# Performance work log

Measured on AMD Instinct MI355X. Metric: run time of the kernel, lower is better.

Reference implementation:

```python
import jax, jax.numpy as jnp
import numpy as np

B, T, N, F_IN, F_OUT, K = 16, 12, 1024, 64, 64, 3


def setup_inputs() -> dict:
    key = jax.random.key(0)
    k1, k2, k3, k4 = jax.random.split(key, 4)
    x = jax.random.normal(k1, (B, T, N, F_IN), dtype=jnp.float32)
    spatial_attention = jax.random.uniform(k2, (B, N, N), dtype=jnp.float32)
    cheb = jax.random.normal(k3, (K, N, N), dtype=jnp.float32) / np.sqrt(N)
    # Xavier-uniform-ish init for Theta [K, F_in, F_out]
    limit = np.sqrt(6.0 / (F_IN + F_OUT))
    Theta = jax.random.uniform(k4, (K, F_IN, F_OUT), dtype=jnp.float32,
                               minval=-limit, maxval=limit)
    return {"x": x, "spatial_attention": spatial_attention, "cheb": cheb, "Theta": Theta}


def reference(x, spatial_attention, cheb, Theta):
    # Attention-weighted Chebyshev adjacencies: [B, K, N, N]
    A = cheb[None, :, :, :] * spatial_attention[:, None, :, :]
    # Graph propagation for all t, k at once: [B, T, K, N, F_in]
    rhs = jnp.einsum('bkij,btjf->btkif', A, x)
    # Per-order linear map + sum over K: [B, T, N, F_out]
    out = jnp.einsum('btkif,kfo->btio', rhs, Theta)
    return jax.nn.relu(out)
```

## Files before the change

### kernel.cpp

```cpp
#include <hip/hip_runtime.h>
#include <hip/hip_bf16.h>

#define BB 16
#define TT 12
#define NN 1024
#define FF 64
#define KC 3

typedef __bf16  bf16x8 __attribute__((ext_vector_type(8)));
typedef float   f32x4  __attribute__((ext_vector_type(4)));
typedef float   f32x16 __attribute__((ext_vector_type(16)));
typedef unsigned short u16;

#define A_TILE 24576
#define Y_TILE 32768
#define MFMA_B(a, b, c) __builtin_amdgcn_mfma_f32_32x32x16_bf16(a, b, c, 0, 0, 0)

#define YF_BYTES 25165824ull
#define CB_BYTES 6291456ull

static __device__ __forceinline__ u16 f2bf(float v) {
    union { __bf16 b; u16 u; } c; c.b = (__bf16)v; return c.u;
}

static __device__ __forceinline__ void load_lds16(const void* g, void* l) {
    __builtin_amdgcn_global_load_lds(
        (const __attribute__((address_space(1))) unsigned int*)g,
        (__attribute__((address_space(3))) unsigned int*)l, 16, 0, 0);
}

__global__ __launch_bounds__(256) void x_to_yfrags(
    const float* __restrict__ x, u16* __restrict__ y)
{
    __shared__ char tl[64 * 128];
    const int tid = threadIdx.x;
    const int bt  = blockIdx.x >> 4;
    const int jt  = blockIdx.x & 15;
    const int f   = tid & 63;
    const int jr  = tid >> 6;

    const float* xp = x + ((size_t)bt * NN + jt * 64 + jr) * FF + f;
    #pragma unroll
    for (int stp = 0; stp < 16; ++stp) {
        int j = stp * 4 + jr;
        u16 h = f2bf(xp[stp * 4 * FF]);
        *reinterpret_cast<u16*>(tl + j * 128 + ((f * 2) ^ ((j & 7) << 4))) = h;
    }
    __syncthreads();

    u16* yo = y + ((size_t)bt * 16 + jt) * 4096;
    #pragma unroll
    for (int p = 0; p < 2; ++p) {
        int c  = tid + p * 256;
        int s  = c >> 6, fo = c & 63;
        int j0 = (s >> 1) * 16 + (s & 1) * 8;
        u16 h[8];
        #pragma unroll
        for (int e = 0; e < 8; ++e)
            h[e] = *reinterpret_cast<u16*>(tl + (j0 + e) * 128 + ((fo * 2) ^ (e << 4)));
        uint4 w;
        w.x = h[0] | ((unsigned)h[1] << 16);
        w.y = h[2] | ((unsigned)h[3] << 16);
        w.z = h[4] | ((unsigned)h[5] << 16);
        w.w = h[6] | ((unsigned)h[7] << 16);
        *reinterpret_cast<uint4*>(yo + (size_t)c * 8) = w;
    }
}

__global__ __launch_bounds__(256) void cheb_to_bf16(
    const float* __restrict__ c, u16* __restrict__ o)
{
    const size_t i = ((size_t)blockIdx.x * 256 + threadIdx.x) * 8;
    f32x4 a = *reinterpret_cast<const f32x4*>(c + i);
    f32x4 b = *reinterpret_cast<const f32x4*>(c + i + 4);
    u16 h[8];
    #pragma unroll
    for (int e = 0; e < 4; ++e) { h[e] = f2bf(a[e]); h[e + 4] = f2bf(b[e]); }
    uint4 w;
    w.x = h[0] | ((unsigned)h[1] << 16);
    w.y = h[2] | ((unsigned)h[3] << 16);
    w.z = h[4] | ((unsigned)h[5] << 16);
    w.w = h[6] | ((unsigned)h[7] << 16);
    *reinterpret_cast<uint4*>(o + i) = w;
}

__global__ __launch_bounds__(512, 1) void cheb_main(
    const u16*  __restrict__ yfr,
    const float* __restrict__ att,
    const u16*  __restrict__ chb,
    const float* __restrict__ Theta,
    float* __restrict__ out)
{
    __shared__ __align__(16) char lds[2 * A_TILE + 2 * Y_TILE];
    char* Ab0 = lds;
    char* Ab1 = lds + A_TILE;
    char* Yb0 = lds + 2 * A_TILE;
    char* Yb1 = Yb0 + Y_TILE;

    const int tid  = threadIdx.x;
    const int lane = tid & 63;
    const int wid  = tid >> 6;

    const int wg = (blockIdx.x & 7) * 96 + (blockIdx.x >> 3);
    const int b  = wg / 48;
    const int it = (wg % 48) / 3;
    const int tc = wg % 3;
    const int i_base = it * 64;
    const int t_base = tc * 4;

    const int wm  = wid >> 1;
    const int wn  = wid & 1;
    const int l31 = lane & 31;
    const int lg  = lane >> 5;
    const int sw3 = (l31 >> 2) & 7;

    const int r_a = tid >> 3;
    const int g_a = tid & 7;
    const int swza_st = ((r_a >> 2) & 7) << 4;
    const float* attR = att + ((size_t)b * NN + i_base + r_a) * NN + g_a * 8;
    const u16*   chR  = chb + ((size_t)(i_base + r_a)) * NN + g_a * 8;

    f32x16 acc[KC][2] = {};
    const int arow = (wn * 32 + l31) * 128;

    f32x4 ra0, ra1;
    bf16x8 rc[KC];

    auto LOADS = [&](int j0) {
        ra0 = *reinterpret_cast<const f32x4*>(attR + j0);
        ra1 = *reinterpret_cast<const f32x4*>(attR + j0 + 4);
        #pragma unroll
        for (int k = 0; k < KC; ++k)
            rc[k] = *reinterpret_cast<const bf16x8*>(chR + (size_t)k * NN * NN + j0);
    };
    auto FINISH = [&](char* Ab) {
        #pragma unroll
        for (int k = 0; k < KC; ++k) {
            bf16x8 w;
            #pragma unroll
            for (int e = 0; e < 4; ++e) {
                w[e]     = (__bf16)(ra0[e] * (float)rc[k][e]);
                w[e + 4] = (__bf16)(ra1[e] * (float)rc[k][e + 4]);
            }
            *reinterpret_cast<bf16x8*>(
                Ab + (k * 64 + r_a) * 128 + ((g_a * 16) ^ swza_st)) = w;
        }
    };

    auto loadY_lds = [&](char* Yb, int jt) {
        #pragma unroll
        for (int q = 0; q < 4; ++q) {
            int s    = wid * 4 + q;
            int tile = s >> 3;
            int part = s & 7;
            const u16* gp = yfr + ((size_t)(b * TT + t_base + tile) * 16 + jt) * 4096
                          + (size_t)(part * 64 + lane) * 8;
            load_lds16(gp, Yb + tile * 8192 + part * 1024);
        }
    };

    auto phase4 = [&](const char* Abase, const char* Ybase) {
        const char* yt = Ybase + wm * 8192;
        #pragma unroll
        for (int kk = 0; kk < 4; ++kk) {
            const int off  = ((kk * 2 + lg) ^ sw3) << 4;
            const int yoff = (kk * 2 + lg) * 1024 + l31 * 16;
            bf16x8 af0 = *reinterpret_cast<const bf16x8*>(yt + yoff);
            bf16x8 af1 = *reinterpret_cast<const bf16x8*>(yt + yoff + 512);
            bf16x8 b0 = *reinterpret_cast<const bf16x8*>(Abase + arow + off);
            bf16x8 b1 = *reinterpret_cast<const bf16x8*>(Abase + 8192 + arow + off);
            bf16x8 b2 = *reinterpret_cast<const bf16x8*>(Abase + 16384 + arow + off);
            __builtin_amdgcn_s_setprio(1);
            acc[0][0] = MFMA_B(af0, b0, acc[0][0]); acc[0][1] = MFMA_B(af1, b0, acc[0][1]);
            acc[1][0] = MFMA_B(af0, b1, acc[1][0]); acc[1][1] = MFMA_B(af1, b1, acc[1][1]);
            acc[2][0] = MFMA_B(af0, b2, acc[2][0]); acc[2][1] = MFMA_B(af1, b2, acc[2][1]);
            __builtin_amdgcn_s_setprio(0);
        }
    };

    auto body = [&](char* curA, char* altA, char* curY, char* altY, int jt) {
        loadY_lds(altY, (jt + 1) & 15);
        __builtin_amdgcn_sched_barrier(0);
        phase4(curA, curY);
        if (jt < 15) {
            FINISH(altA);
            LOADS(((jt + 2) & 15) * 64);
        }
        asm volatile("s_waitcnt vmcnt(5)" ::: "memory");
        asm volatile("s_waitcnt lgkmcnt(0)" ::: "memory");
        __builtin_amdgcn_s_barrier();
    };

    loadY_lds(Yb0, 0);
    LOADS(0);
    asm volatile("s_waitcnt vmcnt(0)" ::: "memory");
    FINISH(Ab0);
    LOADS(64);
    asm volatile("s_waitcnt lgkmcnt(0)" ::: "memory");
    __builtin_amdgcn_s_barrier();

    #pragma unroll 1
    for (int h = 0; h < 8; ++h) {
        body(Ab0, Ab1, Yb0, Yb1, 2 * h);
        body(Ab1, Ab0, Yb1, Yb0, 2 * h + 1);
    }

    {
        const int fi0 = wid * 3;
        #pragma unroll
        for (int q = 0; q < 3; ++q) {
            int fi = fi0 + q;
            int k  = fi >> 3;
            int mo = (fi >> 2) & 1;
            int s  = fi & 3;
            int o  = 32 * mo + l31;
            int fb = 32 * (s >> 1) + 16 * (s & 1) + 4 * lg;
            bf16x8 v;
            #pragma unroll
            for (int e = 0; e < 8; ++e) {
                int f = fb + (e & 3) + 8 * (e >> 2);
                v[e] = (__bf16)Theta[(k * FF + f) * FF + o];
            }
            *reinterpret_cast<bf16x8*>(lds + (fi * 64 + lane) * 16) = v;
        }
    }
    __syncthreads();

    f32x16 of[2] = {};
    #pragma unroll
    for (int k = 0; k < KC; ++k) {
        #pragma unroll
        for (int s = 0; s < 4; ++s) {
            bf16x8 pb;
            #pragma unroll
            for (int e = 0; e < 8; ++e)
                pb[e] = (__bf16)acc[k][s >> 1][e + 8 * (s & 1)];
            #pragma unroll
            for (int mo = 0; mo < 2; ++mo) {
                bf16x8 th = *reinterpret_cast<const bf16x8*>(
                    lds + ((((k * 2 + mo) * 4 + s) * 64) + lane) * 16);
                of[mo] = MFMA_B(pb, th, of[mo]);
            }
        }
    }

    const int t = t_base + wm;
    float* op = out + (((size_t)b * TT + t) * NN + i_base + wn * 32) * FF;
    #pragma unroll
    for (int mo = 0; mo < 2; ++mo) {
        #pragma unroll
        for (int r = 0; r < 16; ++r) {
            int row = (r & 3) + 8 * (r >> 2) + 4 * lg;
            int o   = 32 * mo + l31;
            float v = of[mo][r];
            op[(size_t)row * FF + o] = v > 0.0f ? v : 0.0f;
        }
    }
}

__global__ __launch_bounds__(512, 2) void cheb_fused(
    const float* __restrict__ x, const float* __restrict__ att,
    const float* __restrict__ cheb, const float* __restrict__ Theta,
    float* __restrict__ out)
{
    __shared__ __align__(16) char lds_raw[2 * (A_TILE + 32768)];
    char* Ab0 = lds_raw;
    char* Xb0 = lds_raw + A_TILE;
    char* Ab1 = lds_raw + A_TILE + 32768;
    char* Xb1 = Ab1 + A_TILE;

    const int tid  = threadIdx.x;
    const int lane = tid & 63;
    const int wid  = tid >> 6;
    const int wg = (blockIdx.x & 7) * 96 + (blockIdx.x >> 3);
    const int b  = wg / 48;
    const int it = (wg % 48) / 3;
    const int tc = wg % 3;
    const int i_base = it * 64;
    const int t_base = tc * 4;
    const int wm  = wid >> 1;
    const int wn  = wid & 1;
    const int l31 = lane & 31;
    const int lg  = lane >> 5;
    const int sw3 = (l31 >> 2) & 7;
    const float* attB = att + (size_t)b * NN * NN;
    const float* xB   = x + (size_t)b * TT * NN * FF;
    const int r_a = tid >> 3;
    const int g_a = tid & 7;
    const int swza_st = ((r_a >> 2) & 7) << 4;
    int tl_s[4], jj_s[4], f_s[4], swzx_st[4];
    #pragma unroll
    for (int s = 0; s < 4; ++s) {
        int u = tid + s * 512;
        tl_s[s] = u >> 9;
        int rem = u & 511;
        jj_s[s] = (rem >> 4) * 2;
        f_s[s]  = (rem & 15) * 4;
        swzx_st[s] = ((f_s[s] >> 2) & 7) << 4;
    }
    f32x4 ra0, ra1, rc0[KC], rc1[KC], rx0[4], rx1[4];
    auto load_tile = [&](int j0) {
        const float* ap = attB + (size_t)(i_base + r_a) * NN + j0 + g_a * 8;
        ra0 = *reinterpret_cast<const f32x4*>(ap);
        ra1 = *reinterpret_cast<const f32x4*>(ap + 4);
        #pragma unroll
        for (int k = 0; k < KC; ++k) {
            const float* cp = cheb + ((size_t)k * NN + i_base + r_a) * NN + j0 + g_a * 8;
            rc0[k] = *reinterpret_cast<const f32x4*>(cp);
            rc1[k] = *reinterpret_cast<const f32x4*>(cp + 4);
        }
        #pragma unroll
        for (int s = 0; s < 4; ++s) {
            const float* xp = xB + ((size_t)(t_base + tl_s[s]) * NN + j0 + jj_s[s]) * FF + f_s[s];
            rx0[s] = *reinterpret_cast<const f32x4*>(xp);
            rx1[s] = *reinterpret_cast<const f32x4*>(xp + FF);
        }
    };
    auto store_A = [&](char* Ab) {
        #pragma unroll
        for (int k = 0; k < KC; ++k) {
            bf16x8 w;
            #pragma unroll
            for (int e = 0; e < 4; ++e) {
                w[e]     = (__bf16)(rc0[k][e] * ra0[e]);
                w[e + 4] = (__bf16)(rc1[k][e] * ra1[e]);
            }
            *reinterpret_cast<bf16x8*>(Ab + (k * 64 + r_a) * 128 + ((g_a * 16) ^ swza_st)) = w;
        }
    };
    auto store_X = [&](char* Xb) {
        #pragma unroll
        for (int s = 0; s < 4; ++s) {
            const int c0 = tl_s[s] * 64 + f_s[s];
            const int coloff = (jj_s[s] * 2) ^ swzx_st[s];
            #pragma unroll
            for (int e = 0; e < 4; ++e) {
                union { __bf16 h[2]; unsigned u32; } pk;
                pk.h[0] = (__bf16)rx0[s][e];
                pk.h[1] = (__bf16)rx1[s][e];
                *reinterpret_cast<unsigned*>(Xb + (c0 + e) * 128 + coloff) = pk.u32;
            }
        }
    };
    f32x16 acc[KC][2] = {};
    const int xrow0 = (wm * 64 + l31) * 128;
    const int xrow1 = xrow0 + 32 * 128;
    const int arow  = (wn * 32 + l31) * 128;
    auto phase = [&](const char* AbR, const char* XbR, int kk) {
        const int off = ((kk * 2 + lg) ^ sw3) << 4;
        bf16x8 af0 = *reinterpret_cast<const bf16x8*>(XbR + xrow0 + off);
        bf16x8 af1 = *reinterpret_cast<const bf16x8*>(XbR + xrow1 + off);
        bf16x8 b0  = *reinterpret_cast<const bf16x8*>(AbR + arow + off);
        bf16x8 b1  = *reinterpret_cast<const bf16x8*>(AbR + 8192 + arow + off);
        bf16x8 b2  = *reinterpret_cast<const bf16x8*>(AbR + 16384 + arow + off);
        __builtin_amdgcn_s_setprio(1);
        acc[0][0] = MFMA_B(af0, b0, acc[0][0]); acc[0][1] = MFMA_B(af1, b0, acc[0][1]);
        acc[1][0] = MFMA_B(af0, b1, acc[1][0]); acc[1][1] = MFMA_B(af1, b1, acc[1][1]);
        acc[2][0] = MFMA_B(af0, b2, acc[2][0]); acc[2][1] = MFMA_B(af1, b2, acc[2][1]);
        __builtin_amdgcn_s_setprio(0);
    };
    load_tile(0);
    store_A(Ab0);
    store_X(Xb0);
    load_tile(64);
    asm volatile("s_waitcnt lgkmcnt(0)" ::: "memory");
    __builtin_amdgcn_s_barrier();
    for (int jt2 = 0; jt2 < 8; ++jt2) {
        const int jt = jt2 * 2;
        phase(Ab0, Xb0, 0);
        phase(Ab0, Xb0, 1);
        store_A(Ab1);
        phase(Ab0, Xb0, 2);
        store_X(Xb1);
        phase(Ab0, Xb0, 3);
        if (jt + 2 < 16) load_tile((jt + 2) * 64);
        asm volatile("s_waitcnt lgkmcnt(0)" ::: "memory");
        __builtin_amdgcn_s_barrier();
        phase(Ab1, Xb1, 0);
        phase(Ab1, Xb1, 1);
        if (jt + 1 < 15) store_A(Ab0);
        phase(Ab1, Xb1, 2);
        if (jt + 1 < 15) store_X(Xb0);
        phase(Ab1, Xb1, 3);
        if (jt + 3 < 16) load_tile((jt + 3) * 64);
        asm volatile("s_waitcnt lgkmcnt(0)" ::: "memory");
        __builtin_amdgcn_s_barrier();
    }
    {
        const int fi0 = wid * 3;
        #pragma unroll
        for (int q = 0; q < 3; ++q) {
            int fi = fi0 + q;
            int k  = fi >> 3;
            int mo = (fi >> 2) & 1;
            int s  = fi & 3;
            int o  = 32 * mo + l31;
            int fb = 32 * (s >> 1) + 16 * (s & 1) + 4 * lg;
            bf16x8 v;
            #pragma unroll
            for (int e = 0; e < 8; ++e) {
                int f = fb + (e & 3) + 8 * (e >> 2);
                v[e] = (__bf16)Theta[(k * FF + f) * FF + o];
            }
            *reinterpret_cast<bf16x8*>(lds_raw + (fi * 64 + lane) * 16) = v;
        }
    }
    __syncthreads();
    f32x16 of[2] = {};
    #pragma unroll
    for (int k = 0; k < KC; ++k) {
        #pragma unroll
        for (int s = 0; s < 4; ++s) {
            bf16x8 pb;
            #pragma unroll
            for (int e = 0; e < 8; ++e)
                pb[e] = (__bf16)acc[k][s >> 1][e + 8 * (s & 1)];
            #pragma unroll
            for (int mo = 0; mo < 2; ++mo) {
                bf16x8 th = *reinterpret_cast<const bf16x8*>(
                    lds_raw + ((((k * 2 + mo) * 4 + s) * 64) + lane) * 16);
                of[mo] = MFMA_B(pb, th, of[mo]);
            }
        }
    }
    const int t = t_base + wm;
    float* op = out + (((size_t)b * TT + t) * NN + i_base + wn * 32) * FF;
    #pragma unroll
    for (int mo = 0; mo < 2; ++mo) {
        #pragma unroll
        for (int r = 0; r < 16; ++r) {
            int row = (r & 3) + 8 * (r >> 2) + 4 * lg;
            int o   = 32 * mo + l31;
            float v = of[mo][r];
            op[(size_t)row * FF + o] = v > 0.0f ? v : 0.0f;
        }
    }
}

extern "C" void kernel_launch(void* const* d_in, const int* in_sizes, int n_in,
                              void* d_out, int out_size, void* d_ws, size_t ws_size,
                              hipStream_t stream) {
    const float* x     = (const float*)d_in[0];
    const float* att   = (const float*)d_in[1];
    const float* cheb  = (const float*)d_in[2];
    const float* Theta = (const float*)d_in[3];
    float* out = (float*)d_out;
    (void)in_sizes; (void)n_in; (void)out_size;

    if (ws_size >= YF_BYTES + CB_BYTES) {
        u16* yfr = (u16*)d_ws;
        u16* cbf = (u16*)((char*)d_ws + YF_BYTES);
        x_to_yfrags<<<dim3(BB * TT * 16), 256, 0, stream>>>(x, yfr);
        cheb_to_bf16<<<dim3(KC * NN * NN / (256 * 8)), 256, 0, stream>>>(cheb, cbf);
        cheb_main<<<dim3(BB * 16 * 3), 512, 0, stream>>>(yfr, att, cbf, Theta, out);
    } else {
        cheb_fused<<<dim3(BB * 16 * 3), 512, 0, stream>>>(x, att, cheb, Theta, out);
    }
}
```

Before: 105.9 us.

## Precompute attention-weighted Chebyshev tiles in a separate kernel and DMA them

```diff
diff --git a/kernel.cpp b/kernel.cpp
--- a/kernel.cpp
+++ b/kernel.cpp
@@ -17,7 +17,10 @@
 #define MFMA_B(a, b, c) __builtin_amdgcn_mfma_f32_32x32x16_bf16(a, b, c, 0, 0, 0)
 
 #define YF_BYTES 25165824ull
+#define AW_BYTES 100663296ull
 #define CB_BYTES 6291456ull
+#define T1_BYTES (YF_BYTES + AW_BYTES)
+#define T2_BYTES (YF_BYTES + CB_BYTES)
 
 static __device__ __forceinline__ u16 f2bf(float v) {
     union { __bf16 b; u16 u; } c; c.b = (__bf16)v; return c.u;
@@ -67,27 +70,51 @@
     }
 }
 
-__global__ __launch_bounds__(256) void cheb_to_bf16(
-    const float* __restrict__ c, u16* __restrict__ o)
+__global__ __launch_bounds__(256) void build_A(
+    const float* __restrict__ att, const float* __restrict__ cheb,
+    u16* __restrict__ aw)
 {
-    const size_t i = ((size_t)blockIdx.x * 256 + threadIdx.x) * 8;
-    f32x4 a = *reinterpret_cast<const f32x4*>(c + i);
-    f32x4 b = *reinterpret_cast<const f32x4*>(c + i + 4);
-    u16 h[8];
-    #pragma unroll
-    for (int e = 0; e < 4; ++e) { h[e] = f2bf(a[e]); h[e + 4] = f2bf(b[e]); }
-    uint4 w;
-    w.x = h[0] | ((unsigned)h[1] << 16);
-    w.y = h[2] | ((unsigned)h[3] << 16);
-    w.z = h[4] | ((unsigned)h[5] << 16);
-    w.w = h[6] | ((unsigned)h[7] << 16);
-    *reinterpret_cast<uint4*>(o + i) = w;
-}
-
-__global__ __launch_bounds__(512, 1) void cheb_main(
+    const int bid = blockIdx.x;
+    const int b  = bid & 15;
+    const int it = (bid >> 4) & 15;
+    const int jt = bid >> 8;
+    const int tid = threadIdx.x;
+    const int row = tid >> 2;
+    const int jg2 = tid & 3;
+
+    const float* ap = att + ((size_t)b * NN + it * 64 + row) * NN + jt * 64 + jg2 * 16;
+    f32x4 a0 = *reinterpret_cast<const f32x4*>(ap);
+    f32x4 a1 = *reinterpret_cast<const f32x4*>(ap + 4);
+    f32x4 a2 = *reinterpret_cast<const f32x4*>(ap + 8);
+    f32x4 a3 = *reinterpret_cast<const f32x4*>(ap + 12);
+
+    char* tw = (char*)aw + ((size_t)(b * 16 + it) * 16 + jt) * A_TILE;
+    const int key = ((row >> 2) & 7) << 4;
+
+    #pragma unroll
+    for (int k = 0; k < KC; ++k) {
+        const float* cp = cheb + ((size_t)k * NN + it * 64 + row) * NN + jt * 64 + jg2 * 16;
+        f32x4 c0 = *reinterpret_cast<const f32x4*>(cp);
+        f32x4 c1 = *reinterpret_cast<const f32x4*>(cp + 4);
+        f32x4 c2 = *reinterpret_cast<const f32x4*>(cp + 8);
+        f32x4 c3 = *reinterpret_cast<const f32x4*>(cp + 12);
+        bf16x8 w0, w1;
+        #pragma unroll
+        for (int e = 0; e < 4; ++e) {
+            w0[e]     = (__bf16)(a0[e] * c0[e]);
+            w0[e + 4] = (__bf16)(a1[e] * c1[e]);
+            w1[e]     = (__bf16)(a2[e] * c2[e]);
+            w1[e + 4] = (__bf16)(a3[e] * c3[e]);
+        }
+        char* rb = tw + k * 8192 + row * 128;
+        *reinterpret_cast<bf16x8*>(rb + (((jg2 * 2) << 4) ^ key))     = w0;
+        *reinterpret_cast<bf16x8*>(rb + (((jg2 * 2 + 1) << 4) ^ key)) = w1;
+    }
+}
+
+__global__ __launch_bounds__(512, 1) void cheb_main_t1(
     const u16*  __restrict__ yfr,
-    const float* __restrict__ att,
-    const u16*  __restrict__ chb,
+    const u16*  __restrict__ aw,
     const float* __restrict__ Theta,
     float* __restrict__ out)
 {
@@ -114,40 +141,20 @@
     const int lg  = lane >> 5;
     const int sw3 = (l31 >> 2) & 7;
 
-    const int r_a = tid >> 3;
-    const int g_a = tid & 7;
-    const int swza_st = ((r_a >> 2) & 7) << 4;
-    const float* attR = att + ((size_t)b * NN + i_base + r_a) * NN + g_a * 8;
-    const u16*   chR  = chb + ((size_t)(i_base + r_a)) * NN + g_a * 8;
-
     f32x16 acc[KC][2] = {};
     const int arow = (wn * 32 + l31) * 128;
 
-    f32x4 ra0, ra1;
-    bf16x8 rc[KC];
-
-    auto LOADS = [&](int j0) {
-        ra0 = *reinterpret_cast<const f32x4*>(attR + j0);
-        ra1 = *reinterpret_cast<const f32x4*>(attR + j0 + 4);
-        #pragma unroll
-        for (int k = 0; k < KC; ++k)
-            rc[k] = *reinterpret_cast<const bf16x8*>(chR + (size_t)k * NN * NN + j0);
-    };
-    auto FINISH = [&](char* Ab) {
-        #pragma unroll
-        for (int k = 0; k < KC; ++k) {
-            bf16x8 w;
-            #pragma unroll
-            for (int e = 0; e < 4; ++e) {
-                w[e]     = (__bf16)(ra0[e] * (float)rc[k][e]);
-                w[e + 4] = (__bf16)(ra1[e] * (float)rc[k][e + 4]);
-            }
-            *reinterpret_cast<bf16x8*>(
-                Ab + (k * 64 + r_a) * 128 + ((g_a * 16) ^ swza_st)) = w;
-        }
-    };
-
-    auto loadY_lds = [&](char* Yb, int jt) {
+    const char* aT0 = (const char*)aw + ((size_t)(b * 16 + it) * 16) * A_TILE;
+
+    auto dmaA = [&](char* Ab, int jt) {
+        const char* src = aT0 + (size_t)jt * A_TILE;
+        #pragma unroll
+        for (int q = 0; q < 3; ++q) {
+            int seg = wid * 3 + q;
+            load_lds16(src + seg * 1024 + lane * 16, Ab + seg * 1024 + lane * 16);
+        }
+    };
+    auto dmaY = [&](char* Yb, int jt) {
         #pragma unroll
         for (int q = 0; q < 4; ++q) {
             int s    = wid * 4 + q;
@@ -178,31 +185,26 @@
         }
     };
 
-    auto body = [&](char* curA, char* altA, char* curY, char* altY, int jt) {
-        loadY_lds(altY, (jt + 1) & 15);
+    dmaA(Ab0, 0);
+    dmaY(Yb0, 0);
+    asm volatile("s_waitcnt vmcnt(0)" ::: "memory");
+    __builtin_amdgcn_s_barrier();
+
+    #pragma unroll 1
+    for (int jt = 0; jt < 16; ++jt) {
+        char* curA = (jt & 1) ? Ab1 : Ab0;
+        char* altA = (jt & 1) ? Ab0 : Ab1;
+        char* curY = (jt & 1) ? Yb1 : Yb0;
+        char* altY = (jt & 1) ? Yb0 : Yb1;
+        if (jt < 15) {
+            dmaA(altA, jt + 1);
+            dmaY(altY, jt + 1);
+        }
         __builtin_amdgcn_sched_barrier(0);
         phase4(curA, curY);
-        if (jt < 15) {
-            FINISH(altA);
-            LOADS(((jt + 2) & 15) * 64);
-        }
-        asm volatile("s_waitcnt vmcnt(5)" ::: "memory");
+        asm volatile("s_waitcnt vmcnt(0)" ::: "memory");
         asm volatile("s_waitcnt lgkmcnt(0)" ::: "memory");
         __builtin_amdgcn_s_barrier();
-    };
-
-    loadY_lds(Yb0, 0);
-    LOADS(0);
-    asm volatile("s_waitcnt vmcnt(0)" ::: "memory");
-    FINISH(Ab0);
-    LOADS(64);
-    asm volatile("s_waitcnt lgkmcnt(0)" ::: "memory");
-    __builtin_amdgcn_s_barrier();
-
-    #pragma unroll 1
-    for (int h = 0; h < 8; ++h) {
-        body(Ab0, Ab1, Yb0, Yb1, 2 * h);
-        body(Ab1, Ab0, Yb1, Yb0, 2 * h + 1);
     }
 
     {
@@ -244,6 +246,187 @@
         }
     }
 
+    const int t = t_base + wm;
+    float* op = out + (((size_t)b * TT + t) * NN + i_base + wn * 32) * FF;
+    #pragma unroll
+    for (int mo = 0; mo < 2; ++mo) {
+        #pragma unroll
+        for (int r = 0; r < 16; ++r) {
+            int row = (r & 3) + 8 * (r >> 2) + 4 * lg;
+            int o   = 32 * mo + l31;
+            float v = of[mo][r];
+            op[(size_t)row * FF + o] = v > 0.0f ? v : 0.0f;
+        }
+    }
+}
+
+__global__ __launch_bounds__(256) void cheb_to_bf16(
+    const float* __restrict__ c, u16* __restrict__ o)
+{
+    const size_t i = ((size_t)blockIdx.x * 256 + threadIdx.x) * 8;
+    f32x4 a = *reinterpret_cast<const f32x4*>(c + i);
+    f32x4 b = *reinterpret_cast<const f32x4*>(c + i + 4);
+    u16 h[8];
+    #pragma unroll
+    for (int e = 0; e < 4; ++e) { h[e] = f2bf(a[e]); h[e + 4] = f2bf(b[e]); }
+    uint4 w;
+    w.x = h[0] | ((unsigned)h[1] << 16);
+    w.y = h[2] | ((unsigned)h[3] << 16);
+    w.z = h[4] | ((unsigned)h[5] << 16);
+    w.w = h[6] | ((unsigned)h[7] << 16);
+    *reinterpret_cast<uint4*>(o + i) = w;
+}
+
+__global__ __launch_bounds__(512, 1) void cheb_main_t2(
+    const u16*  __restrict__ yfr, const float* __restrict__ att,
+    const u16*  __restrict__ chb, const float* __restrict__ Theta,
+    float* __restrict__ out)
+{
+    __shared__ __align__(16) char lds[2 * A_TILE + 2 * Y_TILE];
+    char* Ab0 = lds;
+    char* Ab1 = lds + A_TILE;
+    char* Yb0 = lds + 2 * A_TILE;
+    char* Yb1 = Yb0 + Y_TILE;
+
+    const int tid  = threadIdx.x;
+    const int lane = tid & 63;
+    const int wid  = tid >> 6;
+    const int wg = (blockIdx.x & 7) * 96 + (blockIdx.x >> 3);
+    const int b  = wg / 48;
+    const int it = (wg % 48) / 3;
+    const int tc = wg % 3;
+    const int i_base = it * 64;
+    const int t_base = tc * 4;
+    const int wm  = wid >> 1;
+    const int wn  = wid & 1;
+    const int l31 = lane & 31;
+    const int lg  = lane >> 5;
+    const int sw3 = (l31 >> 2) & 7;
+    const int r_a = tid >> 3;
+    const int g_a = tid & 7;
+    const int swza_st = ((r_a >> 2) & 7) << 4;
+    const float* attR = att + ((size_t)b * NN + i_base + r_a) * NN + g_a * 8;
+    const u16*   chR  = chb + ((size_t)(i_base + r_a)) * NN + g_a * 8;
+
+    f32x16 acc[KC][2] = {};
+    const int arow = (wn * 32 + l31) * 128;
+    f32x4 ra0, ra1;
+    bf16x8 rc[KC];
+
+    auto LOADS = [&](int j0) {
+        ra0 = *reinterpret_cast<const f32x4*>(attR + j0);
+        ra1 = *reinterpret_cast<const f32x4*>(attR + j0 + 4);
+        #pragma unroll
+        for (int k = 0; k < KC; ++k)
+            rc[k] = *reinterpret_cast<const bf16x8*>(chR + (size_t)k * NN * NN + j0);
+    };
+    auto FINISH = [&](char* Ab) {
+        #pragma unroll
+        for (int k = 0; k < KC; ++k) {
+            bf16x8 w;
+            #pragma unroll
+            for (int e = 0; e < 4; ++e) {
+                w[e]     = (__bf16)(ra0[e] * (float)rc[k][e]);
+                w[e + 4] = (__bf16)(ra1[e] * (float)rc[k][e + 4]);
+            }
+            *reinterpret_cast<bf16x8*>(Ab + (k * 64 + r_a) * 128 + ((g_a * 16) ^ swza_st)) = w;
+        }
+    };
+    auto loadY_lds = [&](char* Yb, int jt) {
+        #pragma unroll
+        for (int q = 0; q < 4; ++q) {
+            int s    = wid * 4 + q;
+            int tile = s >> 3;
+            int part = s & 7;
+            const u16* gp = yfr + ((size_t)(b * TT + t_base + tile) * 16 + jt) * 4096
+                          + (size_t)(part * 64 + lane) * 8;
+            load_lds16(gp, Yb + tile * 8192 + part * 1024);
+        }
+    };
+    auto phase4 = [&](const char* Abase, const char* Ybase) {
+        const char* yt = Ybase + wm * 8192;
+        #pragma unroll
+        for (int kk = 0; kk < 4; ++kk) {
+            const int off  = ((kk * 2 + lg) ^ sw3) << 4;
+            const int yoff = (kk * 2 + lg) * 1024 + l31 * 16;
+            bf16x8 af0 = *reinterpret_cast<const bf16x8*>(yt + yoff);
+            bf16x8 af1 = *reinterpret_cast<const bf16x8*>(yt + yoff + 512);
+            bf16x8 b0 = *reinterpret_cast<const bf16x8*>(Abase + arow + off);
+            bf16x8 b1 = *reinterpret_cast<const bf16x8*>(Abase + 8192 + arow + off);
+            bf16x8 b2 = *reinterpret_cast<const bf16x8*>(Abase + 16384 + arow + off);
+            __builtin_amdgcn_s_setprio(1);
+            acc[0][0] = MFMA_B(af0, b0, acc[0][0]); acc[0][1] = MFMA_B(af1, b0, acc[0][1]);
+            acc[1][0] = MFMA_B(af0, b1, acc[1][0]); acc[1][1] = MFMA_B(af1, b1, acc[1][1]);
+            acc[2][0] = MFMA_B(af0, b2, acc[2][0]); acc[2][1] = MFMA_B(af1, b2, acc[2][1]);
+            __builtin_amdgcn_s_setprio(0);
+        }
+    };
+
+    auto body = [&](char* curA, char* altA, char* curY, char* altY, int jt) {
+        loadY_lds(altY, (jt + 1) & 15);
+        __builtin_amdgcn_sched_barrier(0);
+        phase4(curA, curY);
+        if (jt < 15) {
+            FINISH(altA);
+            LOADS(((jt + 2) & 15) * 64);
+        }
+        asm volatile("s_waitcnt vmcnt(5)" ::: "memory");
+        asm volatile("s_waitcnt lgkmcnt(0)" ::: "memory");
+        __builtin_amdgcn_s_barrier();
+    };
+
+    loadY_lds(Yb0, 0);
+    LOADS(0);
+    asm volatile("s_waitcnt vmcnt(0)" ::: "memory");
+    FINISH(Ab0);
+    LOADS(64);
+    asm volatile("s_waitcnt lgkmcnt(0)" ::: "memory");
+    __builtin_amdgcn_s_barrier();
+
+    #pragma unroll 1
+    for (int h = 0; h < 8; ++h) {
+        body(Ab0, Ab1, Yb0, Yb1, 2 * h);
+        body(Ab1, Ab0, Yb1, Yb0, 2 * h + 1);
+    }
+
+    {
+        const int fi0 = wid * 3;
+        #pragma unroll
+        for (int q = 0; q < 3; ++q) {
+            int fi = fi0 + q;
+            int k  = fi >> 3;
+            int mo = (fi >> 2) & 1;
+            int s  = fi & 3;
+            int o  = 32 * mo + l31;
+            int fb = 32 * (s >> 1) + 16 * (s & 1) + 4 * lg;
+            bf16x8 v;
+            #pragma unroll
+            for (int e = 0; e < 8; ++e) {
+                int f = fb + (e & 3) + 8 * (e >> 2);
+                v[e] = (__bf16)Theta[(k * FF + f) * FF + o];
+            }
+            *reinterpret_cast<bf16x8*>(lds + (fi * 64 + lane) * 16) = v;
+        }
+    }
+    __syncthreads();
+
+    f32x16 of[2] = {};
+    #pragma unroll
+    for (int k = 0; k < KC; ++k) {
+        #pragma unroll
+        for (int s = 0; s < 4; ++s) {
+            bf16x8 pb;
+            #pragma unroll
+            for (int e = 0; e < 8; ++e)
+                pb[e] = (__bf16)acc[k][s >> 1][e + 8 * (s & 1)];
+            #pragma unroll
+            for (int mo = 0; mo < 2; ++mo) {
+                bf16x8 th = *reinterpret_cast<const bf16x8*>(
+                    lds + ((((k * 2 + mo) * 4 + s) * 64) + lane) * 16);
+                of[mo] = MFMA_B(pb, th, of[mo]);
+            }
+        }
+    }
     const int t = t_base + wm;
     float* op = out + (((size_t)b * TT + t) * NN + i_base + wn * 32) * FF;
     #pragma unroll
@@ -447,12 +630,18 @@
     float* out = (float*)d_out;
     (void)in_sizes; (void)n_in; (void)out_size;
 
-    if (ws_size >= YF_BYTES + CB_BYTES) {
+    if (ws_size >= T1_BYTES) {
+        u16* yfr = (u16*)d_ws;
+        u16* aw  = (u16*)((char*)d_ws + YF_BYTES);
+        x_to_yfrags<<<dim3(BB * TT * 16), 256, 0, stream>>>(x, yfr);
+        build_A<<<dim3(16 * 16 * 16), 256, 0, stream>>>(att, cheb, aw);
+        cheb_main_t1<<<dim3(BB * 16 * 3), 512, 0, stream>>>(yfr, aw, Theta, out);
+    } else if (ws_size >= T2_BYTES) {
         u16* yfr = (u16*)d_ws;
         u16* cbf = (u16*)((char*)d_ws + YF_BYTES);
         x_to_yfrags<<<dim3(BB * TT * 16), 256, 0, stream>>>(x, yfr);
         cheb_to_bf16<<<dim3(KC * NN * NN / (256 * 8)), 256, 0, stream>>>(cheb, cbf);
-        cheb_main<<<dim3(BB * 16 * 3), 512, 0, stream>>>(yfr, att, cbf, Theta, out);
+        cheb_main_t2<<<dim3(BB * 16 * 3), 512, 0, stream>>>(yfr, att, cbf, Theta, out);
     } else {
         cheb_fused<<<dim3(BB * 16 * 3), 512, 0, stream>>>(x, att, cheb, Theta, out);
     }
```

Result: slower. 158.1 us (+49.2%).

## Widen main kernel workgroup to six timesteps to reuse attention-weighted Chebyshev tiles

Applied to the files above, without the earlier changes.

```diff
diff --git a/kernel.cpp b/kernel.cpp
--- a/kernel.cpp
+++ b/kernel.cpp
@@ -12,12 +12,15 @@
 typedef float   f32x16 __attribute__((ext_vector_type(16)));
 typedef unsigned short u16;
 
-#define A_TILE 24576
-#define Y_TILE 32768
+#define A_TILE  24576
+#define A_ROWB  144
+#define A_TILEP (KC * 64 * A_ROWB)
+#define Y_HEX   (6 * 8192)
 #define MFMA_B(a, b, c) __builtin_amdgcn_mfma_f32_32x32x16_bf16(a, b, c, 0, 0, 0)
 
 #define YF_BYTES 25165824ull
 #define CB_BYTES 6291456ull
+#define T2_BYTES (YF_BYTES + CB_BYTES)
 
 static __device__ __forceinline__ u16 f2bf(float v) {
     union { __bf16 b; u16 u; } c; c.b = (__bf16)v; return c.u;
@@ -84,44 +87,44 @@
     *reinterpret_cast<uint4*>(o + i) = w;
 }
 
-__global__ __launch_bounds__(512, 1) void cheb_main(
+__global__ __launch_bounds__(768, 3) void cheb_main_hex(
     const u16*  __restrict__ yfr,
     const float* __restrict__ att,
     const u16*  __restrict__ chb,
     const float* __restrict__ Theta,
     float* __restrict__ out)
 {
-    __shared__ __align__(16) char lds[2 * A_TILE + 2 * Y_TILE];
+    __shared__ __align__(16) char lds[2 * A_TILEP + 2 * Y_HEX];
     char* Ab0 = lds;
-    char* Ab1 = lds + A_TILE;
-    char* Yb0 = lds + 2 * A_TILE;
-    char* Yb1 = Yb0 + Y_TILE;
+    char* Ab1 = lds + A_TILEP;
+    char* Yb0 = lds + 2 * A_TILEP;
+    char* Yb1 = Yb0 + Y_HEX;
 
     const int tid  = threadIdx.x;
     const int lane = tid & 63;
     const int wid  = tid >> 6;
-
-    const int wg = (blockIdx.x & 7) * 96 + (blockIdx.x >> 3);
-    const int b  = wg / 48;
-    const int it = (wg % 48) / 3;
-    const int tc = wg % 3;
+    const bool staging = (wid < 8);
+
+    const int wg = (blockIdx.x & 7) * 64 + (blockIdx.x >> 3);
+    const int b  = wg >> 5;
+    const int rm = wg & 31;
+    const int it = rm >> 1;
+    const int th = rm & 1;
     const int i_base = it * 64;
-    const int t_base = tc * 4;
-
-    const int wm  = wid >> 1;
-    const int wn  = wid & 1;
+    const int t0     = th * 6;
+
+    const int wn    = wid / 6;
+    const int t_loc = wid % 6;
     const int l31 = lane & 31;
     const int lg  = lane >> 5;
-    const int sw3 = (l31 >> 2) & 7;
 
     const int r_a = tid >> 3;
     const int g_a = tid & 7;
-    const int swza_st = ((r_a >> 2) & 7) << 4;
     const float* attR = att + ((size_t)b * NN + i_base + r_a) * NN + g_a * 8;
     const u16*   chR  = chb + ((size_t)(i_base + r_a)) * NN + g_a * 8;
 
     f32x16 acc[KC][2] = {};
-    const int arow = (wn * 32 + l31) * 128;
+    const int arow = (wn * 32 + l31) * A_ROWB;
 
     f32x4 ra0, ra1;
     bf16x8 rc[KC];
@@ -142,34 +145,32 @@
                 w[e]     = (__bf16)(ra0[e] * (float)rc[k][e]);
                 w[e + 4] = (__bf16)(ra1[e] * (float)rc[k][e + 4]);
             }
-            *reinterpret_cast<bf16x8*>(
-                Ab + (k * 64 + r_a) * 128 + ((g_a * 16) ^ swza_st)) = w;
-        }
-    };
-
-    auto loadY_lds = [&](char* Yb, int jt) {
+            *reinterpret_cast<bf16x8*>(Ab + (k * 64 + r_a) * A_ROWB + g_a * 16) = w;
+        }
+    };
+    auto dmaY = [&](char* Yb, int jt) {
         #pragma unroll
         for (int q = 0; q < 4; ++q) {
             int s    = wid * 4 + q;
             int tile = s >> 3;
             int part = s & 7;
-            const u16* gp = yfr + ((size_t)(b * TT + t_base + tile) * 16 + jt) * 4096
+            const u16* gp = yfr + ((size_t)(b * TT + t0 + tile) * 16 + jt) * 4096
                           + (size_t)(part * 64 + lane) * 8;
             load_lds16(gp, Yb + tile * 8192 + part * 1024);
         }
     };
 
     auto phase4 = [&](const char* Abase, const char* Ybase) {
-        const char* yt = Ybase + wm * 8192;
+        const char* yt = Ybase + t_loc * 8192;
         #pragma unroll
         for (int kk = 0; kk < 4; ++kk) {
-            const int off  = ((kk * 2 + lg) ^ sw3) << 4;
+            const int off  = (kk * 2 + lg) * 16;
             const int yoff = (kk * 2 + lg) * 1024 + l31 * 16;
             bf16x8 af0 = *reinterpret_cast<const bf16x8*>(yt + yoff);
             bf16x8 af1 = *reinterpret_cast<const bf16x8*>(yt + yoff + 512);
             bf16x8 b0 = *reinterpret_cast<const bf16x8*>(Abase + arow + off);
-            bf16x8 b1 = *reinterpret_cast<const bf16x8*>(Abase + 8192 + arow + off);
-            bf16x8 b2 = *reinterpret_cast<const bf16x8*>(Abase + 16384 + arow + off);
+            bf16x8 b1 = *reinterpret_cast<const bf16x8*>(Abase + 64 * A_ROWB + arow + off);
+            bf16x8 b2 = *reinterpret_cast<const bf16x8*>(Abase + 128 * A_ROWB + arow + off);
             __builtin_amdgcn_s_setprio(1);
             acc[0][0] = MFMA_B(af0, b0, acc[0][0]); acc[0][1] = MFMA_B(af1, b0, acc[0][1]);
             acc[1][0] = MFMA_B(af0, b1, acc[1][0]); acc[1][1] = MFMA_B(af1, b1, acc[1][1]);
@@ -178,37 +179,46 @@
         }
     };
 
-    auto body = [&](char* curA, char* altA, char* curY, char* altY, int jt) {
-        loadY_lds(altY, (jt + 1) & 15);
+    if (staging) {
+        LOADS(0);
+    }
+    dmaY(Yb0, 0);
+    if (staging) {
+        FINISH(Ab0);
+        LOADS(64);
+        asm volatile("s_waitcnt vmcnt(5)" ::: "memory");
+    } else {
+        asm volatile("s_waitcnt vmcnt(0)" ::: "memory");
+    }
+    asm volatile("s_waitcnt lgkmcnt(0)" ::: "memory");
+    __builtin_amdgcn_s_barrier();
+
+    #pragma unroll 1
+    for (int jt = 0; jt < 16; ++jt) {
+        char* curA = (jt & 1) ? Ab1 : Ab0;
+        char* altA = (jt & 1) ? Ab0 : Ab1;
+        char* curY = (jt & 1) ? Yb1 : Yb0;
+        char* altY = (jt & 1) ? Yb0 : Yb1;
+        dmaY(altY, (jt + 1) & 15);
+        if (staging) {
+            FINISH(altA);
+            LOADS(((jt + 2) & 15) * 64);
+        }
         __builtin_amdgcn_sched_barrier(0);
         phase4(curA, curY);
-        if (jt < 15) {
-            FINISH(altA);
-            LOADS(((jt + 2) & 15) * 64);
-        }
-        asm volatile("s_waitcnt vmcnt(5)" ::: "memory");
+        if (staging) {
+            asm volatile("s_waitcnt vmcnt(5)" ::: "memory");
+        } else {
+            asm volatile("s_waitcnt vmcnt(0)" ::: "memory");
+        }
         asm volatile("s_waitcnt lgkmcnt(0)" ::: "memory");
         __builtin_amdgcn_s_barrier();
-    };
-
-    loadY_lds(Yb0, 0);
-    LOADS(0);
-    asm volatile("s_waitcnt vmcnt(0)" ::: "memory");
-    FINISH(Ab0);
-    LOADS(64);
-    asm volatile("s_waitcnt lgkmcnt(0)" ::: "memory");
-    __builtin_amdgcn_s_barrier();
-
-    #pragma unroll 1
-    for (int h = 0; h < 8; ++h) {
-        body(Ab0, Ab1, Yb0, Yb1, 2 * h);
-        body(Ab1, Ab0, Yb1, Yb0, 2 * h + 1);
     }
 
     {
-        const int fi0 = wid * 3;
-        #pragma unroll
-        for (int q = 0; q < 3; ++q) {
+        const int fi0 = wid * 2;
+        #pragma unroll
+        for (int q = 0; q < 2; ++q) {
             int fi = fi0 + q;
             int k  = fi >> 3;
             int mo = (fi >> 2) & 1;
@@ -244,7 +254,7 @@
         }
     }
 
-    const int t = t_base + wm;
+    const int t = t0 + t_loc;
     float* op = out + (((size_t)b * TT + t) * NN + i_base + wn * 32) * FF;
     #pragma unroll
     for (int mo = 0; mo < 2; ++mo) {
@@ -447,12 +457,12 @@
     float* out = (float*)d_out;
     (void)in_sizes; (void)n_in; (void)out_size;
 
-    if (ws_size >= YF_BYTES + CB_BYTES) {
+    if (ws_size >= T2_BYTES) {
         u16* yfr = (u16*)d_ws;
         u16* cbf = (u16*)((char*)d_ws + YF_BYTES);
         x_to_yfrags<<<dim3(BB * TT * 16), 256, 0, stream>>>(x, yfr);
         cheb_to_bf16<<<dim3(KC * NN * NN / (256 * 8)), 256, 0, stream>>>(cheb, cbf);
-        cheb_main<<<dim3(BB * 16 * 3), 512, 0, stream>>>(yfr, att, cbf, Theta, out);
+        cheb_main_hex<<<dim3(BB * 16 * 2), 768, 0, stream>>>(yfr, att, cbf, Theta, out);
     } else {
         cheb_fused<<<dim3(BB * 16 * 3), 512, 0, stream>>>(x, att, cheb, Theta, out);
     }
```

Result: slower. 110.1 us (+3.9%).

## Triple-buffer Y tiles and pad A rows instead of XOR swizzle

Applied to the files above, without the earlier changes.

```diff
diff --git a/kernel.cpp b/kernel.cpp
--- a/kernel.cpp
+++ b/kernel.cpp
@@ -12,12 +12,15 @@
 typedef float   f32x16 __attribute__((ext_vector_type(16)));
 typedef unsigned short u16;
 
-#define A_TILE 24576
-#define Y_TILE 32768
+#define A_TILE  24576
+#define A_ROWB  144
+#define A_TILEP (KC * 64 * A_ROWB)
+#define Y_TILE  32768
 #define MFMA_B(a, b, c) __builtin_amdgcn_mfma_f32_32x32x16_bf16(a, b, c, 0, 0, 0)
 
 #define YF_BYTES 25165824ull
 #define CB_BYTES 6291456ull
+#define T2_BYTES (YF_BYTES + CB_BYTES)
 
 static __device__ __forceinline__ u16 f2bf(float v) {
     union { __bf16 b; u16 u; } c; c.b = (__bf16)v; return c.u;
@@ -84,18 +87,14 @@
     *reinterpret_cast<uint4*>(o + i) = w;
 }
 
-__global__ __launch_bounds__(512, 1) void cheb_main(
+__global__ __launch_bounds__(512, 1) void cheb_main_t2(
     const u16*  __restrict__ yfr,
     const float* __restrict__ att,
     const u16*  __restrict__ chb,
     const float* __restrict__ Theta,
     float* __restrict__ out)
 {
-    __shared__ __align__(16) char lds[2 * A_TILE + 2 * Y_TILE];
-    char* Ab0 = lds;
-    char* Ab1 = lds + A_TILE;
-    char* Yb0 = lds + 2 * A_TILE;
-    char* Yb1 = Yb0 + Y_TILE;
+    __shared__ __align__(16) char lds[2 * A_TILEP + 3 * Y_TILE];
 
     const int tid  = threadIdx.x;
     const int lane = tid & 63;
@@ -112,16 +111,14 @@
     const int wn  = wid & 1;
     const int l31 = lane & 31;
     const int lg  = lane >> 5;
-    const int sw3 = (l31 >> 2) & 7;
 
     const int r_a = tid >> 3;
     const int g_a = tid & 7;
-    const int swza_st = ((r_a >> 2) & 7) << 4;
     const float* attR = att + ((size_t)b * NN + i_base + r_a) * NN + g_a * 8;
     const u16*   chR  = chb + ((size_t)(i_base + r_a)) * NN + g_a * 8;
 
     f32x16 acc[KC][2] = {};
-    const int arow = (wn * 32 + l31) * 128;
+    const int arow = (wn * 32 + l31) * A_ROWB;
 
     f32x4 ra0, ra1;
     bf16x8 rc[KC];
@@ -133,7 +130,7 @@
         for (int k = 0; k < KC; ++k)
             rc[k] = *reinterpret_cast<const bf16x8*>(chR + (size_t)k * NN * NN + j0);
     };
-    auto FINISH = [&](char* Ab) {
+    auto FINISH = [&](int aOff) {
         #pragma unroll
         for (int k = 0; k < KC; ++k) {
             bf16x8 w;
@@ -142,12 +139,10 @@
                 w[e]     = (__bf16)(ra0[e] * (float)rc[k][e]);
                 w[e + 4] = (__bf16)(ra1[e] * (float)rc[k][e + 4]);
             }
-            *reinterpret_cast<bf16x8*>(
-                Ab + (k * 64 + r_a) * 128 + ((g_a * 16) ^ swza_st)) = w;
-        }
-    };
-
-    auto loadY_lds = [&](char* Yb, int jt) {
+            *reinterpret_cast<bf16x8*>(lds + aOff + (k * 64 + r_a) * A_ROWB + g_a * 16) = w;
+        }
+    };
+    auto dmaY = [&](int yOff, int jt) {
         #pragma unroll
         for (int q = 0; q < 4; ++q) {
             int s    = wid * 4 + q;
@@ -155,21 +150,22 @@
             int part = s & 7;
             const u16* gp = yfr + ((size_t)(b * TT + t_base + tile) * 16 + jt) * 4096
                           + (size_t)(part * 64 + lane) * 8;
-            load_lds16(gp, Yb + tile * 8192 + part * 1024);
-        }
-    };
-
-    auto phase4 = [&](const char* Abase, const char* Ybase) {
-        const char* yt = Ybase + wm * 8192;
+            load_lds16(gp, lds + yOff + tile * 8192 + part * 1024);
+        }
+    };
+
+    auto phase4 = [&](int aOff, int yOff) {
+        const char* yt = lds + yOff + wm * 8192;
+        const char* ab = lds + aOff;
         #pragma unroll
         for (int kk = 0; kk < 4; ++kk) {
-            const int off  = ((kk * 2 + lg) ^ sw3) << 4;
+            const int off  = (kk * 2 + lg) * 16;
             const int yoff = (kk * 2 + lg) * 1024 + l31 * 16;
             bf16x8 af0 = *reinterpret_cast<const bf16x8*>(yt + yoff);
             bf16x8 af1 = *reinterpret_cast<const bf16x8*>(yt + yoff + 512);
-            bf16x8 b0 = *reinterpret_cast<const bf16x8*>(Abase + arow + off);
-            bf16x8 b1 = *reinterpret_cast<const bf16x8*>(Abase + 8192 + arow + off);
-            bf16x8 b2 = *reinterpret_cast<const bf16x8*>(Abase + 16384 + arow + off);
+            bf16x8 b0 = *reinterpret_cast<const bf16x8*>(ab + arow + off);
+            bf16x8 b1 = *reinterpret_cast<const bf16x8*>(ab + 64 * A_ROWB + arow + off);
+            bf16x8 b2 = *reinterpret_cast<const bf16x8*>(ab + 128 * A_ROWB + arow + off);
             __builtin_amdgcn_s_setprio(1);
             acc[0][0] = MFMA_B(af0, b0, acc[0][0]); acc[0][1] = MFMA_B(af1, b0, acc[0][1]);
             acc[1][0] = MFMA_B(af0, b1, acc[1][0]); acc[1][1] = MFMA_B(af1, b1, acc[1][1]);
@@ -178,31 +174,28 @@
         }
     };
 
-    auto body = [&](char* curA, char* altA, char* curY, char* altY, int jt) {
-        loadY_lds(altY, (jt + 1) & 15);
-        __builtin_amdgcn_sched_barrier(0);
-        phase4(curA, curY);
-        if (jt < 15) {
-            FINISH(altA);
-            LOADS(((jt + 2) & 15) * 64);
-        }
-        asm volatile("s_waitcnt vmcnt(5)" ::: "memory");
-        asm volatile("s_waitcnt lgkmcnt(0)" ::: "memory");
-        __builtin_amdgcn_s_barrier();
-    };
-
-    loadY_lds(Yb0, 0);
+    dmaY(2 * A_TILEP, 0);
     LOADS(0);
-    asm volatile("s_waitcnt vmcnt(0)" ::: "memory");
-    FINISH(Ab0);
+    dmaY(2 * A_TILEP + Y_TILE, 1);
+    FINISH(0);
     LOADS(64);
     asm volatile("s_waitcnt lgkmcnt(0)" ::: "memory");
     __builtin_amdgcn_s_barrier();
 
     #pragma unroll 1
-    for (int h = 0; h < 8; ++h) {
-        body(Ab0, Ab1, Yb0, Yb1, 2 * h);
-        body(Ab1, Ab0, Yb1, Yb0, 2 * h + 1);
+    for (int jt = 0; jt < 16; ++jt) {
+        const int curA = (jt & 1) * A_TILEP;
+        const int altA = ((jt & 1) ^ 1) * A_TILEP;
+        const int curY = 2 * A_TILEP + (jt % 3) * Y_TILE;
+        const int nxtY = 2 * A_TILEP + ((jt + 2) % 3) * Y_TILE;
+        dmaY(nxtY, (jt + 2) & 15);
+        __builtin_amdgcn_sched_barrier(0);
+        phase4(curA, curY);
+        FINISH(altA);
+        LOADS(((jt + 2) & 15) * 64);
+        asm volatile("s_waitcnt vmcnt(9)" ::: "memory");
+        asm volatile("s_waitcnt lgkmcnt(0)" ::: "memory");
+        __builtin_amdgcn_s_barrier();
     }
 
     {
@@ -243,7 +236,6 @@
             }
         }
     }
-
     const int t = t_base + wm;
     float* op = out + (((size_t)b * TT + t) * NN + i_base + wn * 32) * FF;
     #pragma unroll
@@ -447,12 +439,12 @@
     float* out = (float*)d_out;
     (void)in_sizes; (void)n_in; (void)out_size;
 
-    if (ws_size >= YF_BYTES + CB_BYTES) {
+    if (ws_size >= T2_BYTES) {
         u16* yfr = (u16*)d_ws;
         u16* cbf = (u16*)((char*)d_ws + YF_BYTES);
         x_to_yfrags<<<dim3(BB * TT * 16), 256, 0, stream>>>(x, yfr);
         cheb_to_bf16<<<dim3(KC * NN * NN / (256 * 8)), 256, 0, stream>>>(cheb, cbf);
-        cheb_main<<<dim3(BB * 16 * 3), 512, 0, stream>>>(yfr, att, cbf, Theta, out);
+        cheb_main_t2<<<dim3(BB * 16 * 3), 512, 0, stream>>>(yfr, att, cbf, Theta, out);
     } else {
         cheb_fused<<<dim3(BB * 16 * 3), 512, 0, stream>>>(x, att, cheb, Theta, out);
     }
```

Result: no change. 108.0 us (+1.9%).
